# Kernel tuning notes

Hardware: AMD Instinct MI355X
Metric: run time of the kernel (lower is better)

## Reference

```python
import jax, jax.numpy as jnp
import numpy as np

N_NODES = 100000
N_EDGES = 1600000
IN_C = 128
OUT_C = 128


def setup_inputs() -> dict:
    key = jax.random.key(0)
    k1, k2, k3, k4 = jax.random.split(key, 4)
    x = jax.random.normal(k1, (N_NODES, IN_C), dtype=jnp.float32)
    W = jax.random.normal(k2, (IN_C, OUT_C), dtype=jnp.float32) * (1.0 / np.sqrt(IN_C))
    b = jax.random.normal(k3, (OUT_C,), dtype=jnp.float32) * 0.02
    edge_index = jax.random.randint(k4, (2, N_EDGES), 0, N_NODES, dtype=jnp.int32)
    return {"x": x, "W": W, "b": b, "edge_index": edge_index}


def reference(x, W, b, edge_index):
    N = x.shape[0]
    # Symmetrize edges: concat(edge_index, flip(edge_index)) as in adj()
    row = jnp.concatenate([edge_index[0], edge_index[1]])  # [2E]
    col = jnp.concatenate([edge_index[1], edge_index[0]])  # [2E]
    w = jnp.ones(row.shape, dtype=x.dtype)
    # gcn_norm with self loops (fill value 1): deg includes self-loop weight
    deg = jax.ops.segment_sum(w, row, num_segments=N) + 1.0
    dinv = jnp.where(deg > 0, jax.lax.rsqrt(deg), 0.0)  # [N]
    # Dense linear projection (bias=False)
    xw = x @ W  # [N, out]
    # SpMM: y[row] += dinv[row]*dinv[col] * xw[col]  (scatter-add == coalesced adj matmul)
    norm = dinv[row] * dinv[col]  # [2E]
    msgs = norm[:, None] * xw[col]  # [2E, out] -- dominant memory traffic
    y = jax.ops.segment_sum(msgs, row, num_segments=N)
    # Self-loop contribution: weight dinv[i]^2
    y = y + (dinv * dinv)[:, None] * xw
    return y + b
```

## Files before the change

kernel.cpp:

```cpp
#include <hip/hip_runtime.h>
#include <math.h>

constexpr int N = 100000;
constexpr int E = 1600000;
constexpr int C = 128;
constexpr int NPB   = 256;
constexpr int NBUCK = (N + NPB - 1) / NPB;
constexpr int CAP   = 9472;
constexpr int ADJ_STRIDE = CAP + NPB * 7;
constexpr int GPAD = 16;

typedef __attribute__((ext_vector_type(8))) short bf16x8;
typedef __attribute__((ext_vector_type(4))) float f32x4;

__device__ inline unsigned f2bf(float f) {
    unsigned u = __float_as_uint(f);
    return (u + 0x7fffu + ((u >> 16) & 1u)) >> 16;
}
__device__ inline unsigned pack2(float lo, float hi) {
    return f2bf(lo) | (f2bf(hi) << 16);
}
__device__ inline float bf_lo(unsigned m) { return __uint_as_float(m << 16); }
__device__ inline float bf_hi(unsigned m) { return __uint_as_float(m & 0xffff0000u); }

__global__ __launch_bounds__(256) void k_bin(const int* __restrict__ ei,
                                             int* __restrict__ gcount,
                                             unsigned* __restrict__ staging,
                                             const float* __restrict__ W,
                                             unsigned short* __restrict__ wfrag,
                                             unsigned* __restrict__ z16) {
    const int t = threadIdx.x;
    if (blockIdx.x < 64) {
        const int i = blockIdx.x * 256 + t;
        const int k = i >> 7, c = i & 127;
        const int ct = c >> 4, lr = c & 15;
        const int kc = k >> 5, lg = (k >> 3) & 3, e = k & 7;
        const int idx = ((ct * 4 + kc) * 64 + lg * 16 + lr) * 8 + e;
        const float f = W[i];
        const unsigned hb = f2bf(f);
        wfrag[idx]         = (unsigned short)hb;
        wfrag[16384 + idx] = (unsigned short)f2bf(f - __uint_as_float(hb << 16));
        if (blockIdx.x == 0 && t < 64) z16[(size_t)N * 64 + t] = 0u;
    }
    __shared__ int cnt[NBUCK];
    const long tile = (long)blockIdx.x * 4096;
    for (int i = t; i < NBUCK; i += 256) cnt[i] = 0;
    __syncthreads();
#pragma unroll
    for (int j = 0; j < 16; ++j) {
        const long e = tile + j * 256 + t;
        if (e < E) {
            const int u = ei[e];
            const int v = ei[E + e];
            atomicAdd(&cnt[u >> 8], 1);
            atomicAdd(&cnt[v >> 8], 1);
        }
    }
    __syncthreads();
    for (int i = t; i < NBUCK; i += 256) {
        const int c = cnt[i];
        cnt[i] = atomicAdd(&gcount[i * GPAD], c);
    }
    __syncthreads();
#pragma unroll
    for (int j = 0; j < 16; ++j) {
        const long e = tile + j * 256 + t;
        if (e < E) {
            const int u = ei[e];
            const int v = ei[E + e];
            const int bu = u >> 8, bv = v >> 8;
            const int pu = atomicAdd(&cnt[bu], 1);
            const int pv = atomicAdd(&cnt[bv], 1);
            staging[(size_t)bu * CAP + pu] = ((unsigned)(u & 255) << 17) | (unsigned)v;
            staging[(size_t)bv * CAP + pv] = ((unsigned)(v & 255) << 17) | (unsigned)u;
        }
    }
}

__global__ __launch_bounds__(512) void k_csr(const unsigned* __restrict__ staging,
                                             const int* __restrict__ gcount,
                                             int* __restrict__ deg,
                                             float* __restrict__ dinv,
                                             int* __restrict__ rowptr,
                                             int* __restrict__ adj) {
    __shared__ int hist[NPB];
    __shared__ int wpart[4];
    const int g = blockIdx.x;
    const int t = threadIdx.x;
    const int lane = t & 63, wid = t >> 6;
    const int cnt = gcount[g * GPAD];
    int* slice = adj + (size_t)g * ADJ_STRIDE;
    for (int i = t; i < NPB; i += 512) hist[i] = 0;
    __syncthreads();
    const unsigned* base = staging + (size_t)g * CAP;
    for (int i = t; i < cnt; i += 512) atomicAdd(&hist[base[i] >> 17], 1);
    __syncthreads();
    const int d  = (t < NPB) ? hist[t] : 0;
    const int pd = (d + 7) & ~7;
    int v = pd;
#pragma unroll
    for (int off = 1; off < 64; off <<= 1) {
        int n = __shfl_up(v, off);
        if (lane >= off) v += n;
    }
    if (lane == 63 && wid < 4) wpart[wid] = v;
    __syncthreads();
    if (t == 0) {
        int r = 0;
#pragma unroll
        for (int w = 0; w < 4; ++w) { int x = wpart[w]; wpart[w] = r; r += x; }
    }
    __syncthreads();
    const int pstart = v - pd + ((wid < 4) ? wpart[wid] : 0);
    if (t < NPB) {
        const int node = g * NPB + t;
        if (node < N) {
            deg[node]    = d;
            dinv[node]   = rsqrtf((float)d + 1.0f);
            rowptr[node] = g * ADJ_STRIDE + pstart;
        }
        for (int i = d; i < pd; ++i) slice[pstart + i] = N;
    }
    __syncthreads();
    if (t < NPB) hist[t] = pstart;
    __syncthreads();
    for (int i = t; i < cnt; i += 512) {
        const unsigned e = base[i];
        const int pos = atomicAdd(&hist[e >> 17], 1);
        slice[pos] = (int)(e & 0x1ffffu);
    }
}

__global__ __launch_bounds__(512) void k_gemm(const float* __restrict__ x,
                                              const unsigned short* __restrict__ wfrag,
                                              const float* __restrict__ dinv,
                                              unsigned* __restrict__ z16) {
    __shared__ unsigned short wlds[32768];
    const int t = threadIdx.x;
    {
        const uint4* src = (const uint4*)wfrag;
        uint4* dst = (uint4*)wlds;
#pragma unroll
        for (int j = 0; j < 8; ++j) dst[t + 512 * j] = src[t + 512 * j];
    }
    __syncthreads();

    const int wid = t >> 6, l = t & 63;
    const int lr = l & 15, lg = l >> 4;
    const unsigned short* wl_hi = wlds + l * 8;
    const unsigned short* wl_lo = wlds + 16384 + l * 8;
    constexpr int NT2 = (N + 127) / 128;

    for (int tile = blockIdx.x; tile < NT2; tile += gridDim.x) {
        const long node = (long)tile * 128 + wid * 16 + lr;
        const bool nv = node < N;
        const float* xr = x + node * C + lg * 8;

        bf16x8 bh[4], bl[4];
#pragma unroll
        for (int kc = 0; kc < 4; ++kc) {
            float4 f0 = {0.f, 0.f, 0.f, 0.f}, f1 = {0.f, 0.f, 0.f, 0.f};
            if (nv) {
                f0 = *(const float4*)(xr + kc * 32);
                f1 = *(const float4*)(xr + kc * 32 + 4);
            }
#pragma unroll
            for (int e = 0; e < 8; ++e) {
                const float fe = (e < 4) ? (&f0.x)[e] : (&f1.x)[e - 4];
                const unsigned hb = f2bf(fe);
                bh[kc][e] = (short)hb;
                bl[kc][e] = (short)f2bf(fe - __uint_as_float(hb << 16));
            }
        }
        const float dv = nv ? dinv[node] : 0.f;

#pragma unroll
        for (int ct = 0; ct < 8; ++ct) {
            f32x4 a = {0.f, 0.f, 0.f, 0.f};
#pragma unroll
            for (int kc = 0; kc < 4; ++kc) {
                const int fo = (ct * 4 + kc) * 512;
                const bf16x8 h = *(const bf16x8*)(wl_hi + fo);
                const bf16x8 o = *(const bf16x8*)(wl_lo + fo);
                a = __builtin_amdgcn_mfma_f32_16x16x32_bf16(h, bh[kc], a, 0, 0, 0);
                a = __builtin_amdgcn_mfma_f32_16x16x32_bf16(h, bl[kc], a, 0, 0, 0);
                a = __builtin_amdgcn_mfma_f32_16x16x32_bf16(o, bh[kc], a, 0, 0, 0);
            }
            if (nv) {
                uint2 pk = {pack2(dv * a[0], dv * a[1]), pack2(dv * a[2], dv * a[3])};
                *(uint2*)(z16 + node * 64 + ct * 8 + lg * 2) = pk;
            }
        }
    }
}

__global__ __launch_bounds__(256) void k_gather(const int* __restrict__ rowptr,
                                                const int* __restrict__ deg,
                                                const float* __restrict__ dinv,
                                                const int* __restrict__ adj,
                                                const unsigned* __restrict__ z16,
                                                const float* __restrict__ b,
                                                float* __restrict__ out,
                                                int u0, int u1) {
    const int u = u0 + blockIdx.x * 4 + (threadIdx.x >> 6);
    if (u >= u1) return;
    const int lane = threadIdx.x & 63;
    const int d  = __builtin_amdgcn_readfirstlane(deg[u]);
    const int pd = (d + 7) & ~7;
    const int st = __builtin_amdgcn_readfirstlane(rowptr[u]);
    const float du = dinv[u];

    const unsigned ms = z16[((size_t)(unsigned)u << 6) + lane];
    float ax = bf_lo(ms), ay = bf_hi(ms);

    unsigned q0, q1, q2, q3, q4, q5, q6, q7;
    unsigned r0, r1, r2, r3, r4, r5, r6, r7;

#define ZR(j) z16[((size_t)(unsigned)__builtin_amdgcn_readlane(v, (j)) << 6) + lane]
#define LD8(A, p) A##0 = ZR((p) + 0); A##1 = ZR((p) + 1); A##2 = ZR((p) + 2); \
                  A##3 = ZR((p) + 3); A##4 = ZR((p) + 4); A##5 = ZR((p) + 5); \
                  A##6 = ZR((p) + 6); A##7 = ZR((p) + 7);
#define AC8(A) ax += bf_lo(A##0); ay += bf_hi(A##0); ax += bf_lo(A##1); ay += bf_hi(A##1); \
               ax += bf_lo(A##2); ay += bf_hi(A##2); ax += bf_lo(A##3); ay += bf_hi(A##3); \
               ax += bf_lo(A##4); ay += bf_hi(A##4); ax += bf_lo(A##5); ay += bf_hi(A##5); \
               ax += bf_lo(A##6); ay += bf_hi(A##6); ax += bf_lo(A##7); ay += bf_hi(A##7);

    for (int j0 = 0; j0 < pd; j0 += 64) {
        const int cntc = min(64, pd - j0);
        const int v = adj[st + j0 + lane];
        int p = 8;
        LD8(q, 0);
        for (; p + 16 <= cntc; p += 16) {
            LD8(r, p); AC8(q);
            LD8(q, p + 8); AC8(r);
        }
        if (p < cntc) { LD8(r, p); AC8(q); AC8(r); }
        else          { AC8(q); }
    }
#undef ZR
#undef LD8
#undef AC8

    const float2 bb = *(const float2*)(b + 2 * lane);
    float2 o = {fmaf(du, ax, bb.x), fmaf(du, ay, bb.y)};
    *(float2*)(out + (size_t)u * C + 2 * lane) = o;
}

extern "C" void kernel_launch(void* const* d_in, const int* in_sizes, int n_in,
                              void* d_out, int out_size, void* d_ws, size_t ws_size,
                              hipStream_t stream) {
    const float* x  = (const float*)d_in[0];
    const float* W  = (const float*)d_in[1];
    const float* b  = (const float*)d_in[2];
    const int*   ei = (const int*)d_in[3];
    float* out = (float*)d_out;

    char* p = (char*)d_ws;
    unsigned* z16 = (unsigned*)p;
    unsigned* staging = z16;
    p += (size_t)(N + 1) * 64 * sizeof(unsigned);
    int* adj = (int*)p;             p += ((size_t)NBUCK * ADJ_STRIDE + 64) * sizeof(int);
    int* deg = (int*)p;             p += (size_t)N * sizeof(int);
    float* dinv = (float*)p;        p += (size_t)N * sizeof(float);
    int* rowptr = (int*)p;          p += (size_t)(N + 4) * sizeof(int);
    int* gcount = (int*)p;          p += (size_t)NBUCK * GPAD * sizeof(int);
    unsigned short* wfrag = (unsigned short*)p;

    hipMemsetAsync(gcount, 0, (size_t)NBUCK * GPAD * sizeof(int), stream);
    k_bin<<<(E + 4095) / 4096, 256, 0, stream>>>(ei, gcount, staging, W, wfrag, z16);
    k_csr<<<NBUCK, 512, 0, stream>>>(staging, gcount, deg, dinv, rowptr, adj);
    k_gemm<<<512, 512, 0, stream>>>(x, wfrag, dinv, z16);
    const int third = (N + 2) / 3;
    for (int s = 0; s < 3; ++s) {
        const int u0 = s * third;
        const int u1 = (u0 + third < N) ? (u0 + third) : N;
        k_gather<<<(u1 - u0 + 3) / 4, 256, 0, stream>>>(rowptr, deg, dinv, adj, z16, b, out, u0, u1);
    }
}
```

Before: 330.9 us.

## Drop LDS staging of W in GEMM, read fragments from global per wave

The GEMM kernel no longer copies the 64 KB split-bf16 weight fragments into shared memory. Each 64-thread wave now handles one 16-node tile and reads W fragments straight from global memory, which should hit in L2 or L1 cache. The grid becomes one wave per tile with 256-thread blocks instead of a persistent grid-stride loop. The goal is to remove the per-block LDS fill and barrier and to raise occupancy by freeing LDS, at the cost of repeated global or cache reads of W and a non-unrolled column loop.

After: 299.0 us. 9.6% less time.

```diff
diff --git a/kernel.cpp b/kernel.cpp
--- a/kernel.cpp
+++ b/kernel.cpp
@@ -131,66 +131,47 @@
     }
 }
 
-__global__ __launch_bounds__(512) void k_gemm(const float* __restrict__ x,
+__global__ __launch_bounds__(256) void k_gemm(const float* __restrict__ x,
                                               const unsigned short* __restrict__ wfrag,
                                               const float* __restrict__ dinv,
                                               unsigned* __restrict__ z16) {
-    __shared__ unsigned short wlds[32768];
-    const int t = threadIdx.x;
-    {
-        const uint4* src = (const uint4*)wfrag;
-        uint4* dst = (uint4*)wlds;
-#pragma unroll
-        for (int j = 0; j < 8; ++j) dst[t + 512 * j] = src[t + 512 * j];
-    }
-    __syncthreads();
-
-    const int wid = t >> 6, l = t & 63;
+    const int g = blockIdx.x * 4 + (threadIdx.x >> 6);
+    if (g >= N / 16) return;
+    const int l  = threadIdx.x & 63;
     const int lr = l & 15, lg = l >> 4;
-    const unsigned short* wl_hi = wlds + l * 8;
-    const unsigned short* wl_lo = wlds + 16384 + l * 8;
-    constexpr int NT2 = (N + 127) / 128;
-
-    for (int tile = blockIdx.x; tile < NT2; tile += gridDim.x) {
-        const long node = (long)tile * 128 + wid * 16 + lr;
-        const bool nv = node < N;
-        const float* xr = x + node * C + lg * 8;
-
-        bf16x8 bh[4], bl[4];
+    const int node = g * 16 + lr;
+    const float* xr = x + (size_t)node * C + lg * 8;
+
+    bf16x8 bh[4], bl[4];
+#pragma unroll
+    for (int kc = 0; kc < 4; ++kc) {
+        const float4 f0 = *(const float4*)(xr + kc * 32);
+        const float4 f1 = *(const float4*)(xr + kc * 32 + 4);
+#pragma unroll
+        for (int e = 0; e < 8; ++e) {
+            const float fe = (e < 4) ? (&f0.x)[e] : (&f1.x)[e - 4];
+            const unsigned hb = f2bf(fe);
+            bh[kc][e] = (short)hb;
+            bl[kc][e] = (short)f2bf(fe - __uint_as_float(hb << 16));
+        }
+    }
+    const float dv = dinv[node];
+    const unsigned short* wl = wfrag + l * 8;
+
+#pragma unroll 1
+    for (int ct = 0; ct < 8; ++ct) {
+        f32x4 a = {0.f, 0.f, 0.f, 0.f};
 #pragma unroll
         for (int kc = 0; kc < 4; ++kc) {
-            float4 f0 = {0.f, 0.f, 0.f, 0.f}, f1 = {0.f, 0.f, 0.f, 0.f};
-            if (nv) {
-                f0 = *(const float4*)(xr + kc * 32);
-                f1 = *(const float4*)(xr + kc * 32 + 4);
-            }
-#pragma unroll
-            for (int e = 0; e < 8; ++e) {
-                const float fe = (e < 4) ? (&f0.x)[e] : (&f1.x)[e - 4];
-                const unsigned hb = f2bf(fe);
-                bh[kc][e] = (short)hb;
-                bl[kc][e] = (short)f2bf(fe - __uint_as_float(hb << 16));
-            }
-        }
-        const float dv = nv ? dinv[node] : 0.f;
-
-#pragma unroll
-        for (int ct = 0; ct < 8; ++ct) {
-            f32x4 a = {0.f, 0.f, 0.f, 0.f};
-#pragma unroll
-            for (int kc = 0; kc < 4; ++kc) {
-                const int fo = (ct * 4 + kc) * 512;
-                const bf16x8 h = *(const bf16x8*)(wl_hi + fo);
-                const bf16x8 o = *(const bf16x8*)(wl_lo + fo);
-                a = __builtin_amdgcn_mfma_f32_16x16x32_bf16(h, bh[kc], a, 0, 0, 0);
-                a = __builtin_amdgcn_mfma_f32_16x16x32_bf16(h, bl[kc], a, 0, 0, 0);
-                a = __builtin_amdgcn_mfma_f32_16x16x32_bf16(o, bh[kc], a, 0, 0, 0);
-            }
-            if (nv) {
-                uint2 pk = {pack2(dv * a[0], dv * a[1]), pack2(dv * a[2], dv * a[3])};
-                *(uint2*)(z16 + node * 64 + ct * 8 + lg * 2) = pk;
-            }
-        }
+            const int fo = (ct * 4 + kc) * 512;
+            const bf16x8 h = *(const bf16x8*)(wl + fo);
+            const bf16x8 o = *(const bf16x8*)(wl + 16384 + fo);
+            a = __builtin_amdgcn_mfma_f32_16x16x32_bf16(h, bh[kc], a, 0, 0, 0);
+            a = __builtin_amdgcn_mfma_f32_16x16x32_bf16(h, bl[kc], a, 0, 0, 0);
+            a = __builtin_amdgcn_mfma_f32_16x16x32_bf16(o, bh[kc], a, 0, 0, 0);
+        }
+        uint2 pk = {pack2(dv * a[0], dv * a[1]), pack2(dv * a[2], dv * a[3])};
+        *(uint2*)(z16 + (size_t)node * 64 + ct * 8 + lg * 2) = pk;
     }
 }
 
@@ -269,7 +250,7 @@
     hipMemsetAsync(gcount, 0, (size_t)NBUCK * GPAD * sizeof(int), stream);
     k_bin<<<(E + 4095) / 4096, 256, 0, stream>>>(ei, gcount, staging, W, wfrag, z16);
     k_csr<<<NBUCK, 512, 0, stream>>>(staging, gcount, deg, dinv, rowptr, adj);
-    k_gemm<<<512, 512, 0, stream>>>(x, wfrag, dinv, z16);
+    k_gemm<<<(N / 16 + 3) / 4, 256, 0, stream>>>(x, wfrag, dinv, z16);
     const int third = (N + 2) / 3;
     for (int s = 0; s < 3; ++s) {
         const int u0 = s * third;
```
